# Optimization experiments

Hardware: AMD Instinct MI355X
Metric: run time of the kernel (lower is better)

The kernel has to match this reference:

```python
import jax, jax.numpy as jnp
import numpy as np

HID = 512
ALPHA = 0.01
PI = np.float32(np.pi)


def _mlp(x, W0, b0, W1, b1, W2, b2, W3, b3):
    # x: [..., 2] -> scalar field u(x): [...]
    h = jnp.tanh(x @ W0 + b0)
    h = jnp.tanh(h @ W1 + b1)
    h = jnp.tanh(h @ W2 + b2)
    return (h @ W3 + b3)[..., 0]


def _forcing(x):
    # f = -Delta u for u = sin(pi x) sin(pi y^2)
    xx, yy = x[:, 0], x[:, 1]
    return (-PI ** 2 * (1 + 4 * yy ** 2) * jnp.sin(PI * xx) * jnp.sin(PI * yy ** 2)
            + 2 * PI * jnp.sin(PI * xx) * jnp.cos(PI * yy ** 2))


def setup_inputs() -> dict:
    key = jax.random.key(0)
    ks = jax.random.split(key, 6)
    n_i, n_b = 20000, 800
    x_interior = jax.random.uniform(ks[0], (n_i, 2), dtype=jnp.float32)  # domain (0,1)
    theta = jnp.linspace(0.0, 2.0 * np.pi, n_b)
    x_boundary = jnp.stack([(jnp.cos(theta) + 1.0) * 0.5,
                            (jnp.sin(theta) + 1.0) * 0.5], axis=1).astype(jnp.float32)

    def w(k, shape, fan_in):
        return (jax.random.normal(k, shape, jnp.float32) / np.float32(np.sqrt(fan_in)))

    W0 = w(ks[1], (2, HID), 2)
    b0 = jnp.zeros((HID,), jnp.float32)
    W1 = w(ks[2], (HID, HID), HID)
    b1 = jnp.zeros((HID,), jnp.float32)
    W2 = w(ks[3], (HID, HID), HID)
    b2 = jnp.zeros((HID,), jnp.float32)
    W3 = w(ks[4], (HID, 1), HID)
    b3 = jnp.zeros((1,), jnp.float32)
    return dict(x_interior=x_interior, x_boundary=x_boundary,
                W0=W0, b0=b0, W1=W1, b1=b1, W2=W2, b2=b2, W3=W3, b3=b3)


def reference(x_interior, x_boundary, W0, b0, W1, b1, W2, b2, W3, b3):
    params = (W0, b0, W1, b1, W2, b2, W3, b3)

    def u_scalar(x):  # x: [2] -> scalar
        return _mlp(x, *params)

    g = jax.grad(u_scalar)

    def lap_one(x):
        # Laplacian = trace of Hessian via forward-over-reverse HVPs
        lap = jnp.float32(0.0)
        for i in range(2):
            e = jnp.zeros((2,), x.dtype).at[i].set(1.0)
            _, hv = jax.jvp(g, (x,), (e,))
            lap = lap + hv[i]
        return lap

    laplacian = jax.vmap(lap_one)(x_interior)  # [n_interior]
    interior_loss = jnp.mean((laplacian - _forcing(x_interior)) ** 2)
    boundary_loss = jnp.mean(_mlp(x_boundary, *params) ** 2)
    total_loss = ALPHA * interior_loss + boundary_loss
    return total_loss, interior_loss, boundary_loss
```

## Files before the change

### kernel.cpp

```cpp
#include <hip/hip_runtime.h>
#include <math.h>

#define HID 512
#define PPB 32
#define SLAB 512

typedef __attribute__((ext_vector_type(8))) _Float16 half8;
typedef __attribute__((ext_vector_type(4))) _Float16 half4;
typedef __attribute__((ext_vector_type(4))) float f32x4;

static __device__ __forceinline__ float fast_tanh(float x) {
    float e = __expf(2.f * x);
    return 1.f - 2.f / (e + 1.f);
}


__global__ __launch_bounds__(256) void prep_wt(
    const float* __restrict__ W1, const float* __restrict__ W2,
    _Float16* __restrict__ W1h, _Float16* __restrict__ W2h)
{
    __shared__ float T[64][65];
    int b = blockIdx.x;
    const float* W = (b < 64) ? W1 : W2;
    _Float16* Wh   = (b < 64) ? W1h : W2h;
    int tb = b & 63;
    int jbG = tb >> 3, kbG = tb & 7;
    int j0 = jbG * 64, k0 = kbG * 64;
    int t = threadIdx.x;
    #pragma unroll
    for (int r = 0; r < 16; ++r) {
        int kl = r * 4 + (t >> 6);
        int jl = t & 63;
        T[kl][jl] = W[(size_t)(k0 + kl) * HID + j0 + jl];
    }
    __syncthreads();
    int ljb = t >> 6;
    int l15 = (t >> 2) & 15;
    int quad = t & 3;
    #pragma unroll
    for (int lkb = 0; lkb < 2; ++lkb) {
        half8 v;
        #pragma unroll
        for (int k8 = 0; k8 < 8; ++k8)
            v[k8] = (_Float16)T[lkb * 32 + quad * 8 + k8][ljb * 16 + l15];
        size_t out = (size_t)((jbG * 4 + ljb) * 16 + (kbG * 2 + lkb)) * SLAB
                   + (quad * 16 + l15) * 8;
        *(half8*)(Wh + out) = v;
    }
}

template<bool FULL>
static __device__ __forceinline__ void layer_pass(
    const _Float16* __restrict__ Wh, const float* __restrict__ bias,
    _Float16* Als, int wv, int lane)
{
    const int l15 = lane & 15, quad = lane >> 4;
    const int j0w = wv * 32;
    const int jb0 = wv * 2;
    const int loff = lane * 8;

    f32x4 acc[4][2][2];
    #pragma unroll
    for (int s = 0; s < 4; ++s)
        #pragma unroll
        for (int pf = 0; pf < 2; ++pf)
            #pragma unroll
            for (int jt = 0; jt < 2; ++jt) acc[s][pf][jt] = (f32x4)0.f;

    half8 wA[2], wB[2];
    #pragma unroll
    for (int jt = 0; jt < 2; ++jt)
        wA[jt] = *(const half8*)(Wh + (size_t)((jb0 + jt) * 16) * SLAB + loff);

    auto iter = [&](int kb, half8 (&wc)[2], half8 (&wn)[2]) {
        if (kb < 15) {
            #pragma unroll
            for (int jt = 0; jt < 2; ++jt)
                wn[jt] = *(const half8*)(Wh + (size_t)((jb0 + jt) * 16 + kb + 1) * SLAB + loff);
        }
        #pragma unroll
        for (int pf = 0; pf < 2; ++pf) {
            half8 a[4];
            #pragma unroll
            for (int s = 0; s < 4; ++s)
                a[s] = *(const half8*)(Als + ((s * 2 + pf) * 16 + kb) * SLAB + loff);
            #pragma unroll
            for (int s = 0; s < 4; ++s)
                #pragma unroll
                for (int jt = 0; jt < 2; ++jt)
                    acc[s][pf][jt] = __builtin_amdgcn_mfma_f32_16x16x32_f16(
                        wc[jt], a[s], acc[s][pf][jt], 0, 0, 0);
        }
    };

    #pragma unroll
    for (int kb = 0; kb < 16; kb += 2) {
        iter(kb,     wA, wB);
        iter(kb + 1, wB, wA);
    }

    __syncthreads();

    #pragma unroll
    for (int jt = 0; jt < 2; ++jt) {
        const int jbase = j0w + jt * 16 + quad * 4;
        const int qo = jt * 2 + (quad >> 1);
        const int e0 = (quad & 1) * 4;
        f32x4 bv = *(const f32x4*)&bias[jbase];
        #pragma unroll
        for (int pf = 0; pf < 2; ++pf) {
            half4 vh, vt1, vt2, vS;
            #pragma unroll
            for (int r = 0; r < 4; ++r) {
                float a  = fast_tanh(acc[0][pf][jt][r] + bv[r]);
                float g  = 1.f - a * a;
                float z1 = acc[1][pf][jt][r];
                float z2 = acc[2][pf][jt][r];
                vh[r] = (_Float16)a;
                if (FULL) {
                    vt1[r] = (_Float16)(g * z1);
                    vt2[r] = (_Float16)(g * z2);
                }
                vS[r] = (_Float16)(g * acc[3][pf][jt][r] - 2.f * a * g * (z1 * z1 + z2 * z2));
            }
            const int ooff = (qo * 16 + l15) * 8 + e0;
            *(half4*)(Als + ((0 * 2 + pf) * 16 + wv) * SLAB + ooff) = vh;
            if (FULL) {
                *(half4*)(Als + ((1 * 2 + pf) * 16 + wv) * SLAB + ooff) = vt1;
                *(half4*)(Als + ((2 * 2 + pf) * 16 + wv) * SLAB + ooff) = vt2;
            }
            *(half4*)(Als + ((3 * 2 + pf) * 16 + wv) * SLAB + ooff) = vS;
        }
    }
    __syncthreads();
}

__global__ __launch_bounds__(1024, 4) void pois_fused(
    const float* __restrict__ x_int, const float* __restrict__ x_bnd,
    const float* __restrict__ W0, const float* __restrict__ b0,
    const _Float16* __restrict__ W1h, const float* __restrict__ b1,
    const _Float16* __restrict__ W2h, const float* __restrict__ b2,
    const float* __restrict__ W3, const float* __restrict__ b3,
    float* __restrict__ partials, int NI, int NT, int nblk)
{
    __shared__ _Float16 Als[8 * 16 * SLAB];
    __shared__ float scU[16][32], scL[16][32], sc[64];

    const int tid = threadIdx.x;
    const int wv = tid >> 6, lane = tid & 63;
    const int l15 = lane & 15, quad = lane >> 4;
    const int p0 = blockIdx.x * PPB;

    #pragma unroll
    for (int ph = 0; ph < 2; ++ph) {
        const int p = ph * 16 + l15;
        int gp = p0 + p;
        int gpc = (gp >= NT) ? 0 : gp;
        float xx, yy;
        if (gpc < NI) { xx = x_int[2 * gpc];        yy = x_int[2 * gpc + 1]; }
        else          { xx = x_bnd[2 * (gpc - NI)]; yy = x_bnd[2 * (gpc - NI) + 1]; }
        const int k = wv * 32 + quad * 8;
        f32x4 w0a = *(const f32x4*)&W0[k],       w0b = *(const f32x4*)&W0[k + 4];
        f32x4 w1a = *(const f32x4*)&W0[HID + k], w1b = *(const f32x4*)&W0[HID + k + 4];
        f32x4 b0a = *(const f32x4*)&b0[k],       b0b = *(const f32x4*)&b0[k + 4];
        half8 vh, vt1, vt2, vS;
        #pragma unroll
        for (int e = 0; e < 8; ++e) {
            float w0i = (e < 4) ? w0a[e] : w0b[e - 4];
            float w1i = (e < 4) ? w1a[e] : w1b[e - 4];
            float bbi = (e < 4) ? b0a[e] : b0b[e - 4];
            float a = fast_tanh(xx * w0i + yy * w1i + bbi);
            float g = 1.f - a * a;
            vh[e]  = (_Float16)a;
            vt1[e] = (_Float16)(g * w0i);
            vt2[e] = (_Float16)(g * w1i);
            vS[e]  = (_Float16)(-2.f * a * g * (w0i * w0i + w1i * w1i));
        }
        const int off = lane * 8;
        *(half8*)(Als + ((0 * 2 + ph) * 16 + wv) * SLAB + off) = vh;
        *(half8*)(Als + ((1 * 2 + ph) * 16 + wv) * SLAB + off) = vt1;
        *(half8*)(Als + ((2 * 2 + ph) * 16 + wv) * SLAB + off) = vt2;
        *(half8*)(Als + ((3 * 2 + ph) * 16 + wv) * SLAB + off) = vS;
    }
    __syncthreads();

    layer_pass<true >(W1h, b1, Als, wv, lane);
    layer_pass<false>(W2h, b2, Als, wv, lane);

    {
        const int k = wv * 32 + quad * 8;
        f32x4 wa = *(const f32x4*)&W3[k], wb = *(const f32x4*)&W3[k + 4];
        #pragma unroll
        for (int ph = 0; ph < 2; ++ph) {
            half8 hh = *(const half8*)(Als + ((0 * 2 + ph) * 16 + wv) * SLAB + lane * 8);
            half8 ss = *(const half8*)(Als + ((3 * 2 + ph) * 16 + wv) * SLAB + lane * 8);
            float u = 0.f, lap = 0.f;
            #pragma unroll
            for (int e = 0; e < 4; ++e) {
                u   += (float)hh[e] * wa[e] + (float)hh[e + 4] * wb[e];
                lap += (float)ss[e] * wa[e] + (float)ss[e + 4] * wb[e];
            }
            u   += __shfl_xor(u, 16);   u   += __shfl_xor(u, 32);
            lap += __shfl_xor(lap, 16); lap += __shfl_xor(lap, 32);
            if (lane < 16) { scU[wv][ph * 16 + lane] = u; scL[wv][ph * 16 + lane] = lap; }
        }
    }
    __syncthreads();
    if (tid < 32) {
        const int p = tid;
        float u = 0.f, lap = 0.f;
        #pragma unroll
        for (int w = 0; w < 16; ++w) { u += scU[w][p]; lap += scL[w][p]; }
        int gp = p0 + p;
        float vi = 0.f, vb = 0.f;
        if (gp < NI) {
            const float PIf = 3.14159265358979323846f;
            float xx = x_int[2 * gp], yy = x_int[2 * gp + 1];
            float sx = sinf(PIf * xx);
            float y2 = yy * yy;
            float sy = sinf(PIf * y2), cy = cosf(PIf * y2);
            float f = -PIf * PIf * (1.f + 4.f * y2) * sx * sy + 2.f * PIf * sx * cy;
            float r = lap - f;
            vi = r * r;
        } else if (gp < NT) {
            float uu = u + b3[0];
            vb = uu * uu;
        }
        sc[p * 2] = vi; sc[p * 2 + 1] = vb;
    }
    __syncthreads();
    if (tid == 0) {
        float svi = 0.f, svb = 0.f;
        #pragma unroll
        for (int p = 0; p < PPB; ++p) { svi += sc[p * 2]; svb += sc[p * 2 + 1]; }
        partials[blockIdx.x] = svi;
        partials[nblk + blockIdx.x] = svb;
    }
}

__global__ __launch_bounds__(256) void pois_reduce(
    const float* __restrict__ partials, float* __restrict__ out,
    int nblk, int NI, int NB)
{
    int tid = threadIdx.x;
    float si = 0.f, sb = 0.f;
    for (int i = tid; i < nblk; i += 256) {
        si += partials[i];
        sb += partials[nblk + i];
    }
    #pragma unroll
    for (int off = 32; off > 0; off >>= 1) {
        si += __shfl_xor(si, off);
        sb += __shfl_xor(sb, off);
    }
    __shared__ float ri[4], rb[4];
    int wv = tid >> 6;
    if ((tid & 63) == 0) { ri[wv] = si; rb[wv] = sb; }
    __syncthreads();
    if (tid == 0) {
        float inter = (ri[0] + ri[1] + ri[2] + ri[3]) / (float)NI;
        float bound = (rb[0] + rb[1] + rb[2] + rb[3]) / (float)NB;
        out[0] = 0.01f * inter + bound;
        out[1] = inter;
        out[2] = bound;
    }
}

extern "C" void kernel_launch(void* const* d_in, const int* in_sizes, int n_in,
                              void* d_out, int out_size, void* d_ws, size_t ws_size,
                              hipStream_t stream)
{
    const float* x_int = (const float*)d_in[0];
    const float* x_bnd = (const float*)d_in[1];
    const float* W0 = (const float*)d_in[2];
    const float* b0 = (const float*)d_in[3];
    const float* W1 = (const float*)d_in[4];
    const float* b1 = (const float*)d_in[5];
    const float* W2 = (const float*)d_in[6];
    const float* b2 = (const float*)d_in[7];
    const float* W3 = (const float*)d_in[8];
    const float* b3 = (const float*)d_in[9];

    int NI = in_sizes[0] / 2;
    int NB = in_sizes[1] / 2;
    int NT = NI + NB;
    int nblk = (NT + PPB - 1) / PPB;

    float* partials = (float*)d_ws;
    _Float16* W1h = (_Float16*)((char*)d_ws + 16384);
    _Float16* W2h = W1h + 262144;

    prep_wt<<<128, 256, 0, stream>>>(W1, W2, W1h, W2h);

    pois_fused<<<nblk, 1024, 0, stream>>>(
        x_int, x_bnd, W0, b0, W1h, b1, W2h, b2, W3, b3,
        partials, NI, NT, nblk);

    pois_reduce<<<1, 256, 0, stream>>>(partials, (float*)d_out, nblk, NI, NB);
}
```

Baseline: 173.7 us.

## Repartition layer MFMA work so each wave owns one point half and 64 outputs

Changes the per-wave work split in the hidden-layer pass. Each of the 16 waves previously covered both point halves for 32 output neurons. Now each wave covers one point half for 64 output neurons. This halves the LDS activation reads per wave per k-step but doubles the global/L2 weight fragment loads, and the output write-back indexing is remapped to match. It shifts pressure from LDS bandwidth toward weight-load bandwidth while keeping the same accumulator register count.

Measured after the change: 345.7 us. +99.0%, slower.

```diff
diff --git a/kernel.cpp b/kernel.cpp
--- a/kernel.cpp
+++ b/kernel.cpp
@@ -55,42 +55,39 @@
     _Float16* Als, int wv, int lane)
 {
     const int l15 = lane & 15, quad = lane >> 4;
-    const int j0w = wv * 32;
-    const int jb0 = wv * 2;
+    const int pf  = wv & 1;
+    const int jg  = wv >> 1;
+    const int j0w = jg * 64;
+    const int jb0 = jg * 4;
     const int loff = lane * 8;
 
-    f32x4 acc[4][2][2];
+    f32x4 acc[4][4];
     #pragma unroll
     for (int s = 0; s < 4; ++s)
         #pragma unroll
-        for (int pf = 0; pf < 2; ++pf)
-            #pragma unroll
-            for (int jt = 0; jt < 2; ++jt) acc[s][pf][jt] = (f32x4)0.f;
-
-    half8 wA[2], wB[2];
-    #pragma unroll
-    for (int jt = 0; jt < 2; ++jt)
+        for (int jt = 0; jt < 4; ++jt) acc[s][jt] = (f32x4)0.f;
+
+    half8 wA[4], wB[4];
+    #pragma unroll
+    for (int jt = 0; jt < 4; ++jt)
         wA[jt] = *(const half8*)(Wh + (size_t)((jb0 + jt) * 16) * SLAB + loff);
 
-    auto iter = [&](int kb, half8 (&wc)[2], half8 (&wn)[2]) {
+    auto iter = [&](int kb, half8 (&wc)[4], half8 (&wn)[4]) {
+        half8 a[4];
+        #pragma unroll
+        for (int s = 0; s < 4; ++s)
+            a[s] = *(const half8*)(Als + ((s * 2 + pf) * 16 + kb) * SLAB + loff);
         if (kb < 15) {
             #pragma unroll
-            for (int jt = 0; jt < 2; ++jt)
+            for (int jt = 0; jt < 4; ++jt)
                 wn[jt] = *(const half8*)(Wh + (size_t)((jb0 + jt) * 16 + kb + 1) * SLAB + loff);
         }
         #pragma unroll
-        for (int pf = 0; pf < 2; ++pf) {
-            half8 a[4];
+        for (int s = 0; s < 4; ++s)
             #pragma unroll
-            for (int s = 0; s < 4; ++s)
-                a[s] = *(const half8*)(Als + ((s * 2 + pf) * 16 + kb) * SLAB + loff);
-            #pragma unroll
-            for (int s = 0; s < 4; ++s)
-                #pragma unroll
-                for (int jt = 0; jt < 2; ++jt)
-                    acc[s][pf][jt] = __builtin_amdgcn_mfma_f32_16x16x32_f16(
-                        wc[jt], a[s], acc[s][pf][jt], 0, 0, 0);
-        }
+            for (int jt = 0; jt < 4; ++jt)
+                acc[s][jt] = __builtin_amdgcn_mfma_f32_16x16x32_f16(
+                    wc[jt], a[s], acc[s][jt], 0, 0, 0);
     };
 
     #pragma unroll
@@ -102,35 +99,34 @@
     __syncthreads();
 
     #pragma unroll
-    for (int jt = 0; jt < 2; ++jt) {
-        const int jbase = j0w + jt * 16 + quad * 4;
-        const int qo = jt * 2 + (quad >> 1);
-        const int e0 = (quad & 1) * 4;
+    for (int jt = 0; jt < 4; ++jt) {
+        const int jo = jt * 16 + quad * 4;
+        const int jbase = j0w + jo;
+        const int okb = jbase >> 5;
+        const int qo  = (jo & 31) >> 3;
+        const int e0  = (quad & 1) * 4;
         f32x4 bv = *(const f32x4*)&bias[jbase];
-        #pragma unroll
-        for (int pf = 0; pf < 2; ++pf) {
-            half4 vh, vt1, vt2, vS;
-            #pragma unroll
-            for (int r = 0; r < 4; ++r) {
-                float a  = fast_tanh(acc[0][pf][jt][r] + bv[r]);
-                float g  = 1.f - a * a;
-                float z1 = acc[1][pf][jt][r];
-                float z2 = acc[2][pf][jt][r];
-                vh[r] = (_Float16)a;
-                if (FULL) {
-                    vt1[r] = (_Float16)(g * z1);
-                    vt2[r] = (_Float16)(g * z2);
-                }
-                vS[r] = (_Float16)(g * acc[3][pf][jt][r] - 2.f * a * g * (z1 * z1 + z2 * z2));
+        half4 vh, vt1, vt2, vS;
+        #pragma unroll
+        for (int r = 0; r < 4; ++r) {
+            float a  = fast_tanh(acc[0][jt][r] + bv[r]);
+            float g  = 1.f - a * a;
+            float z1 = acc[1][jt][r];
+            float z2 = acc[2][jt][r];
+            vh[r] = (_Float16)a;
+            if (FULL) {
+                vt1[r] = (_Float16)(g * z1);
+                vt2[r] = (_Float16)(g * z2);
             }
-            const int ooff = (qo * 16 + l15) * 8 + e0;
-            *(half4*)(Als + ((0 * 2 + pf) * 16 + wv) * SLAB + ooff) = vh;
-            if (FULL) {
-                *(half4*)(Als + ((1 * 2 + pf) * 16 + wv) * SLAB + ooff) = vt1;
-                *(half4*)(Als + ((2 * 2 + pf) * 16 + wv) * SLAB + ooff) = vt2;
-            }
-            *(half4*)(Als + ((3 * 2 + pf) * 16 + wv) * SLAB + ooff) = vS;
-        }
+            vS[r] = (_Float16)(g * acc[3][jt][r] - 2.f * a * g * (z1 * z1 + z2 * z2));
+        }
+        const int ooff = (qo * 16 + l15) * 8 + e0;
+        *(half4*)(Als + ((0 * 2 + pf) * 16 + okb) * SLAB + ooff) = vh;
+        if (FULL) {
+            *(half4*)(Als + ((1 * 2 + pf) * 16 + okb) * SLAB + ooff) = vt1;
+            *(half4*)(Als + ((2 * 2 + pf) * 16 + okb) * SLAB + ooff) = vt2;
+        }
+        *(half4*)(Als + ((3 * 2 + pf) * 16 + okb) * SLAB + ooff) = vS;
     }
     __syncthreads();
 }
```
